# Kernel optimization log

Measured on AMD Instinct MI355X. Metric: run time of the kernel, lower is better.

## Reference

```python
import jax, jax.numpy as jnp
import numpy as np

SLOPE = 0.2  # leaky_relu_slope for both LVC block and kernel predictor (passed through)
DILATIONS = (1, 3, 9, 27)
HOP = 256
STRIDE = 8
IN_CH = 32
KSZ = 3  # conv_kernel_size


def conv1d(x, w, b, dilation=1, padding=0):
    # x: (B,C,T), w: (O,I,K) torch layout
    y = jax.lax.conv_general_dilated(
        x, w, window_strides=(1,), padding=[(padding, padding)],
        rhs_dilation=(dilation,), dimension_numbers=('NCH', 'OIH', 'NCH'))
    return y + b[None, :, None]


def conv_transpose1d(x, w, b, stride, padding, output_padding=0):
    # w: torch ConvTranspose1d layout (Cin, Cout, K)
    w_ = jnp.flip(w, -1).transpose(1, 0, 2)  # (Cout, Cin, K)
    K = w.shape[2]
    pad = (K - 1 - padding, K - 1 - padding + output_padding)
    y = jax.lax.conv_general_dilated(
        x, w_, window_strides=(1,), padding=[pad],
        lhs_dilation=(stride,), dimension_numbers=('NCH', 'OIH', 'NCH'))
    return y + b[None, :, None]


def lrelu(x, slope=SLOPE):
    return jnp.where(x >= 0, x, slope * x)


def location_variable_convolution(x, kernel, bias, hop):
    # x: (B,C,T), kernel: (B,C,O,k,L), bias: (B,O,L); T == L*hop; dilation==1 path
    B, C, T = x.shape
    _, _, O, k, L = kernel.shape
    pad = (k - 1) // 2
    xp = jnp.pad(x, ((0, 0), (0, 0), (pad, pad)))
    # gather per-segment sliding windows: (L, hop, k) index into time axis
    idx = (jnp.arange(L)[:, None, None] * hop
           + jnp.arange(hop)[None, :, None]
           + jnp.arange(k)[None, None, :])
    xw = xp[:, :, idx]  # (B, C, L, hop, k)
    o = jnp.einsum('bclsk,bcokl->bols', xw, kernel)  # (B, O, L, hop)
    o = o + bias[:, :, :, None]
    return o.reshape(B, O, L * hop)


def kernel_predictor(spec, kp_in_w, kp_in_b, rb_w1, rb_b1, rb_w2, rb_b2,
                     kern_w, kern_b, bias_w, bias_b):
    B, _, L = spec.shape
    h = conv1d(spec, kp_in_w, kp_in_b, padding=2)  # k=5, pad=2
    for i in range(3):  # num_blocks = 3
        r = h
        h = conv1d(h, rb_w1[i], rb_b1[i], padding=1)
        h = lrelu(h)
        h = conv1d(h, rb_w2[i], rb_b2[i], padding=1)
        h = lrelu(h) + r
    kh = conv1d(h, kern_w, kern_b, padding=1)
    bh = conv1d(h, bias_w, bias_b, padding=1)
    n_layers = len(DILATIONS)
    kernels = kh.reshape(B, n_layers, IN_CH, 2 * IN_CH, KSZ, L)
    biases = bh.reshape(B, n_layers, 2 * IN_CH, L)
    return kernels, biases


def reference(hidden_states, spectrogram, convt_w, convt_b, kp_in_w, kp_in_b,
              rb_w1, rb_b1, rb_w2, rb_b2, kern_w, kern_b, bias_w, bias_b,
              lvc_w, lvc_b):
    h = conv_transpose1d(hidden_states, convt_w, convt_b,
                         stride=STRIDE, padding=STRIDE // 2 + STRIDE % 2,
                         output_padding=STRIDE % 2)
    kernels, biases = kernel_predictor(spectrogram, kp_in_w, kp_in_b,
                                       rb_w1, rb_b1, rb_w2, rb_b2,
                                       kern_w, kern_b, bias_w, bias_b)
    for i, d in enumerate(DILATIONS):
        r = h
        h = lrelu(h)
        h = conv1d(h, lvc_w[i], lvc_b[i], dilation=d, padding=d * (KSZ - 1) // 2)
        h = lrelu(h)
        h = location_variable_convolution(h, kernels[:, i], biases[:, i], HOP)
        h = jax.nn.sigmoid(h[:, :IN_CH, :]) * jnp.tanh(h[:, IN_CH:, :]) + r
    return h


def setup_inputs() -> dict:
    key = jax.random.key(0)
    ks = jax.random.split(key, 12)
    B, COND, L, H = 4, 100, 256, 64
    T = L * HOP  # 65536 output samples
    s = jnp.float32(0.02)
    d = {}
    d['hidden_states'] = jax.random.normal(ks[0], (B, IN_CH, T // STRIDE), jnp.float32)
    d['spectrogram'] = jax.random.normal(ks[1], (B, COND, L), jnp.float32)
    d['convt_w'] = jax.random.normal(ks[2], (IN_CH, IN_CH, 2 * STRIDE), jnp.float32) * s
    d['convt_b'] = jnp.zeros((IN_CH,), jnp.float32)
    d['kp_in_w'] = jax.random.normal(ks[3], (H, COND, 5), jnp.float32) * s
    d['kp_in_b'] = jnp.zeros((H,), jnp.float32)
    d['rb_w1'] = jax.random.normal(ks[4], (3, H, H, 3), jnp.float32) * s
    d['rb_b1'] = jnp.zeros((3, H), jnp.float32)
    d['rb_w2'] = jax.random.normal(ks[5], (3, H, H, 3), jnp.float32) * s
    d['rb_b2'] = jnp.zeros((3, H), jnp.float32)
    KC = IN_CH * 2 * IN_CH * KSZ * len(DILATIONS)  # 24576
    d['kern_w'] = jax.random.normal(ks[6], (KC, H, 3), jnp.float32) * s
    d['kern_b'] = jnp.zeros((KC,), jnp.float32)
    BC = 2 * IN_CH * len(DILATIONS)  # 256
    d['bias_w'] = jax.random.normal(ks[7], (BC, H, 3), jnp.float32) * s
    d['bias_b'] = jnp.zeros((BC,), jnp.float32)
    d['lvc_w'] = jax.random.normal(ks[8], (len(DILATIONS), IN_CH, IN_CH, 3), jnp.float32) * s
    d['lvc_b'] = jnp.zeros((len(DILATIONS), IN_CH), jnp.float32)
    return d
```

## Files before the change

kernel.cpp:

```cpp
#include <hip/hip_runtime.h>
#include <math.h>

#define NB 4
#define T 65536
#define TIN 8192
#define LL 256
#define KCL 6144

__device__ __forceinline__ float lrelu_f(float v) { return v >= 0.f ? v : 0.2f * v; }

union Phase1LDS {
    struct { float xs[32][264]; float wm[64][128]; } cvt;
    struct { float hs[64][56]; float xsp[20][56]; float wt[192][68]; } trk;
};

__global__ void __launch_bounds__(512) phase1(
    const float* __restrict__ x, const float* __restrict__ cw,
    const float* __restrict__ cbias, float* __restrict__ hout,
    const float* __restrict__ spec,
    const float* __restrict__ kp_in_w, const float* __restrict__ kp_in_b,
    const float* __restrict__ rb_w1, const float* __restrict__ rb_b1,
    const float* __restrict__ rb_w2, const float* __restrict__ rb_b2,
    float* __restrict__ kp_h) {
    __shared__ Phase1LDS u;
    const int bid = blockIdx.x;
    const int tid = threadIdx.x;
    const int lane = tid & 63, wv = tid >> 6;

    if (bid < 264) {
        const int bx = bid % 33;
        const int rr = bid / 33;
        const int mtp = rr & 1;
        const int b = rr >> 1;
        const int s0base = bx * 256;
        float (*xs)[264] = u.cvt.xs;
        float (*wm)[128] = u.cvt.wm;

        const float* xb = x + (size_t)b * 32 * TIN;
        for (int idx = tid; idx < 32 * 64; idx += 512) {
            int c = idx >> 6, q = idx & 63;
            int p = s0base + q * 4;
            float4 v = (p + 3 < TIN) ? *(const float4*)(xb + c * TIN + p)
                                     : make_float4(0.f, 0.f, 0.f, 0.f);
            *(float4*)&xs[c][4 + 4 * q] = v;
        }
        if (tid < 32) {
            int p = s0base - 1;
            xs[tid][3] = (p >= 0) ? xb[tid * TIN + p] : 0.f;
        }
        for (int idx = tid; idx < 8192; idx += 512) {
            int i = idx >> 7, mm = idx & 127;
            int oo = mtp * 16 + (mm >> 3), k0 = mm & 7;
            wm[i][mm] = (i < 32) ? cw[i * 512 + oo * 16 + k0]
                                 : cw[(i - 32) * 512 + oo * 16 + k0 + 8];
        }
        __syncthreads();

        float acc[2][8][4];
#pragma unroll
        for (int ol = 0; ol < 2; ++ol) {
            float bo = cbias[mtp * 16 + wv * 2 + ol];
#pragma unroll
            for (int k0 = 0; k0 < 8; ++k0)
#pragma unroll
                for (int si = 0; si < 4; ++si) acc[ol][k0][si] = bo;
        }

        for (int c = 0; c < 32; ++c) {
            float xm1[4], x0[4];
#pragma unroll
            for (int si = 0; si < 4; ++si) {
                xm1[si] = xs[c][lane + si * 64 + 3];
                x0[si]  = xs[c][lane + si * 64 + 4];
            }
            float w0[16], w1[16];
#pragma unroll
            for (int q = 0; q < 4; ++q) {
                *(float4*)&w0[q * 4] = *(const float4*)&wm[c][wv * 16 + q * 4];
                *(float4*)&w1[q * 4] = *(const float4*)&wm[32 + c][wv * 16 + q * 4];
            }
#pragma unroll
            for (int ol = 0; ol < 2; ++ol)
#pragma unroll
                for (int k0 = 0; k0 < 8; ++k0)
#pragma unroll
                    for (int si = 0; si < 4; ++si)
                        acc[ol][k0][si] += x0[si] * w0[ol * 8 + k0] + xm1[si] * w1[ol * 8 + k0];
        }

#pragma unroll
        for (int ol = 0; ol < 2; ++ol) {
            float* ob = hout + ((size_t)b * 32 + mtp * 16 + wv * 2 + ol) * T;
#pragma unroll
            for (int si = 0; si < 4; ++si) {
                int tb = (s0base + lane + si * 64) * 8 - 4;
                if (tb >= 0 && tb < T)
                    *(float4*)(ob + tb) = make_float4(acc[ol][0][si], acc[ol][1][si],
                                                      acc[ol][2][si], acc[ol][3][si]);
                if (tb + 4 >= 0 && tb + 4 < T)
                    *(float4*)(ob + tb + 4) = make_float4(acc[ol][4][si], acc[ol][5][si],
                                                          acc[ol][6][si], acc[ol][7][si]);
            }
        }
        return;
    }

    const int tb = bid - 264;
    const int lq = tb & 7, b = tb >> 3;
    const int j = lane;
    const int oc0 = wv * 8;
    const int l0 = lq * 32;
    const int labs = l0 - 9 + j;
    const bool lvalid = (labs >= 0 && labs < 256);

    float (*hs)[56] = u.trk.hs;
    float (*xsp)[56] = u.trk.xsp;
    float (*wt)[68] = u.trk.wt;

    float pw[24];
    float px[3];

    auto pf_kpin = [&](int cc) {
#pragma unroll
        for (int t = 0; t < 13; ++t) {
            int idx = t * 512 + tid;
            pw[t] = 0.f;
            if (idx < 6400) pw[t] = kp_in_w[(size_t)(idx / 100) * 500 + cc * 100 + (idx % 100)];
        }
    };
    auto wr_kpin = [&]() {
#pragma unroll
        for (int t = 0; t < 13; ++t) {
            int idx = t * 512 + tid;
            if (idx < 6400) wt[idx % 100][idx / 100] = pw[t];
        }
    };
    auto pf_xsp = [&](int cc) {
#pragma unroll
        for (int t = 0; t < 3; ++t) {
            int idx = t * 512 + tid;
            px[t] = 0.f;
            if (idx < 1120) {
                int c = idx / 56, jj = idx - c * 56;
                int l = l0 - 9 + jj;
                if (l >= 0 && l < 256)
                    px[t] = spec[((size_t)b * 100 + cc * 20 + c) * LL + l];
            }
        }
    };
    auto wr_xsp = [&]() {
#pragma unroll
        for (int t = 0; t < 3; ++t) {
            int idx = t * 512 + tid;
            if (idx < 1120) xsp[idx / 56][idx % 56] = px[t];
        }
    };
    auto pf_w192 = [&](const float* src) {
#pragma unroll
        for (int t = 0; t < 24; ++t) pw[t] = src[t * 512 + tid];
    };
    auto wr_w192 = [&]() {
#pragma unroll
        for (int t = 0; t < 24; ++t) {
            int idx = t * 512 + tid;
            wt[idx % 192][idx / 192] = pw[t];
        }
    };
    auto conv64 = [&](int jlo, int jhi, const float* bptr, float* a) {
#pragma unroll
        for (int oi = 0; oi < 8; ++oi) a[oi] = bptr[oc0 + oi];
        if (j >= jlo && j < jhi) {
            for (int c = 0; c < 64; ++c) {
                float x0 = hs[c][j - 1], x1 = hs[c][j], x2 = hs[c][j + 1];
#pragma unroll
                for (int k = 0; k < 3; ++k) {
                    float xk = (k == 0) ? x0 : (k == 1) ? x1 : x2;
                    float w8[8];
                    *(float4*)&w8[0] = *(const float4*)&wt[c * 3 + k][oc0];
                    *(float4*)&w8[4] = *(const float4*)&wt[c * 3 + k][oc0 + 4];
#pragma unroll
                    for (int oi = 0; oi < 8; ++oi) a[oi] += xk * w8[oi];
                }
            }
        }
    };

    pf_kpin(0); pf_xsp(0);
    wr_kpin(); wr_xsp();
    __syncthreads();

    float acc[8];
#pragma unroll
    for (int oi = 0; oi < 8; ++oi) acc[oi] = kp_in_b[oc0 + oi];

    for (int cc = 0; cc < 5; ++cc) {
        if (cc < 4) { pf_kpin(cc + 1); pf_xsp(cc + 1); }
        else        { pf_w192(rb_w1); }
        if (j >= 2 && j < 48) {
            for (int c = 0; c < 20; ++c) {
                float x5[5];
#pragma unroll
                for (int u2 = 0; u2 < 5; ++u2) x5[u2] = xsp[c][j - 2 + u2];
#pragma unroll
                for (int k = 0; k < 5; ++k) {
                    float w8[8];
                    *(float4*)&w8[0] = *(const float4*)&wt[c * 5 + k][oc0];
                    *(float4*)&w8[4] = *(const float4*)&wt[c * 5 + k][oc0 + 4];
#pragma unroll
                    for (int oi = 0; oi < 8; ++oi) acc[oi] += x5[k] * w8[oi];
                }
            }
        }
        if (cc == 4 && j >= 2 && j < 48) {
#pragma unroll
            for (int oi = 0; oi < 8; ++oi) hs[oc0 + oi][j] = lvalid ? acc[oi] : 0.f;
        }
        __syncthreads();
        if (cc < 4) { wr_kpin(); wr_xsp(); }
        else        { wr_w192(); }
        __syncthreads();
    }

    for (int i = 0; i < 3; ++i) {
        const int jlo1 = 3 + 2 * i, jhi1 = 47 - 2 * i;
        const int jlo2 = jlo1 + 1, jhi2 = jhi1 - 1;
        float r[8];
        if (j >= jlo2 && j < jhi2) {
#pragma unroll
            for (int oi = 0; oi < 8; ++oi) r[oi] = hs[oc0 + oi][j];
        }
        pf_w192(rb_w2 + (size_t)i * 12288);
        float a1[8];
        conv64(jlo1, jhi1, rb_b1 + i * 64, a1);
        __syncthreads();
        if (j >= jlo1 && j < jhi1) {
#pragma unroll
            for (int oi = 0; oi < 8; ++oi) hs[oc0 + oi][j] = lvalid ? lrelu_f(a1[oi]) : 0.f;
        }
        wr_w192();
        __syncthreads();
        if (i < 2) pf_w192(rb_w1 + (size_t)(i + 1) * 12288);
        float a2[8];
        conv64(jlo2, jhi2, rb_b2 + i * 64, a2);
        __syncthreads();
        if (j >= jlo2 && j < jhi2) {
#pragma unroll
            for (int oi = 0; oi < 8; ++oi) hs[oc0 + oi][j] = lvalid ? (lrelu_f(a2[oi]) + r[oi]) : 0.f;
        }
        if (i < 2) wr_w192();
        __syncthreads();
    }

    for (int idx = tid; idx < 64 * 32; idx += 512) {
        int c = idx >> 5, jj = idx & 31;
        kp_h[((size_t)b * 64 + c) * LL + l0 + jj] = hs[c][9 + jj];
    }
}

__global__ void __launch_bounds__(256, 3) kern_head(const float* __restrict__ kp_h,
                                                    const float* __restrict__ kw,
                                                    const float* __restrict__ kb,
                                                    const float* __restrict__ bias_w,
                                                    const float* __restrict__ bias_b,
                                                    float* __restrict__ kh,
                                                    float* __restrict__ bh, int layer) {
    const int bx = blockIdx.x, b = blockIdx.y;
    const bool isbias = (bx >= 192);
    const int tid = threadIdx.x, lane = tid & 63, wv = tid >> 6;
    __shared__ float xs[32][264];
    __shared__ float ws[96][36];

    int g = 0, oc0 = 0, ci = 0, kk = 0, ocb0 = 0;
    const float* wsrc;
    size_t wrow0;
    int wstride;
    if (!isbias) {
        g = bx >> 1; oc0 = (bx & 1) * 32;
        ci = g / 3; kk = g - ci * 3;
        wsrc = kw + (size_t)layer * KCL * 192;
        wrow0 = (size_t)((ci * 64 + oc0) * 3 + kk) * 192;
        wstride = 576;
    } else {
        ocb0 = (bx - 192) * 32;
        wsrc = bias_w;
        wrow0 = (size_t)ocb0 * 192;
        wstride = 192;
    }

    float acc[8][4];
#pragma unroll
    for (int oi = 0; oi < 8; ++oi) {
        float bv = isbias ? bias_b[ocb0 + wv * 8 + oi]
                          : kb[layer * KCL + (ci * 64 + oc0 + wv * 8 + oi) * 3 + kk];
#pragma unroll
        for (int si = 0; si < 4; ++si) acc[oi][si] = bv;
    }

    for (int half = 0; half < 2; ++half) {
        const int hc0 = half * 32;
        __syncthreads();
        for (int idx = tid; idx < 32 * 64; idx += 256) {
            int c = idx >> 6, q = idx & 63;
            *(float4*)&xs[c][4 + 4 * q] =
                *(const float4*)(kp_h + ((size_t)b * 64 + hc0 + c) * LL + 4 * q);
        }
        if (tid < 32) { xs[tid][3] = 0.f; xs[tid][260] = 0.f; }
        for (int idx = tid; idx < 3072; idx += 256) {
            int ocl = idx / 96, jj = idx - ocl * 96;
            ws[jj][ocl] = wsrc[wrow0 + (size_t)ocl * wstride + hc0 * 3 + jj];
        }
        __syncthreads();
        for (int c = 0; c < 32; ++c) {
#pragma unroll
            for (int t = 0; t < 3; ++t) {
                float wv8[8];
                *(float4*)&wv8[0] = *(const float4*)&ws[c * 3 + t][wv * 8];
                *(float4*)&wv8[4] = *(const float4*)&ws[c * 3 + t][wv * 8 + 4];
                float xv[4];
#pragma unroll
                for (int si = 0; si < 4; ++si) xv[si] = xs[c][lane + si * 64 + t + 3];
#pragma unroll
                for (int oi = 0; oi < 8; ++oi)
#pragma unroll
                    for (int si = 0; si < 4; ++si)
                        acc[oi][si] += wv8[oi] * xv[si];
            }
        }
    }

    if (!isbias) {
#pragma unroll
        for (int si = 0; si < 4; ++si) {
            int l = lane + si * 64;
            float* op = kh + ((size_t)b * LL + l) * KCL + g * 64 + oc0 + wv * 8;
            *(float4*)(op)     = make_float4(acc[0][si], acc[1][si], acc[2][si], acc[3][si]);
            *(float4*)(op + 4) = make_float4(acc[4][si], acc[5][si], acc[6][si], acc[7][si]);
        }
    } else {
#pragma unroll
        for (int oi = 0; oi < 8; ++oi) {
            float* op = bh + ((size_t)b * 256 + ocb0 + wv * 8 + oi) * LL;
#pragma unroll
            for (int si = 0; si < 4; ++si)
                op[lane + si * 64] = acc[oi][si];
        }
    }
}

__global__ void __launch_bounds__(512, 4) layer_fused(
    const float* __restrict__ kh, const float* __restrict__ bh,
    const float* __restrict__ w, const float* __restrict__ bias,
    const float* __restrict__ hin, float* __restrict__ hout,
    int layer, int dil) {
    const int l = blockIdx.x, b = blockIdx.y;
    const int tid = threadIdx.x, lane = tid & 63, wv = tid >> 6;
    const int t0 = l * 256;
    __shared__ float xh[32][316];
    __shared__ float ks[KCL];
    __shared__ float ws[96][36];

    const float* hb = hin + (size_t)b * 32 * T;
    for (int idx = tid; idx < 32 * 64; idx += 512) {
        int c = idx >> 6, q = idx & 63;
        float4 v = *(const float4*)(hb + (size_t)c * T + t0 + 4 * q);
        *(float4*)&xh[c][32 + 4 * q] = make_float4(lrelu_f(v.x), lrelu_f(v.y),
                                                   lrelu_f(v.z), lrelu_f(v.w));
    }
    for (int idx = tid; idx < 32 * 60; idx += 512) {
        int c = idx / 60, r = idx - c * 60;
        int jj = (r < 32) ? r : (256 + r);
        int t = t0 + jj - 32;
        xh[c][jj] = (t >= 0 && t < T) ? lrelu_f(hb[(size_t)c * T + t]) : 0.f;
    }
    {
        const float4* kp = (const float4*)(kh + ((size_t)b * LL + l) * KCL);
        float4* kd = (float4*)ks;
        for (int idx = tid; idx < KCL / 4; idx += 512) kd[idx] = kp[idx];
    }
    for (int idx = tid; idx < 3072; idx += 512) {
        int oc = idx / 96, ck = idx - oc * 96;
        ws[ck][oc] = w[oc * 96 + ck];
    }
    __syncthreads();

    const int oc4 = wv * 4;
    float yv[5][4];
    {
        float a[5][4];
#pragma unroll
        for (int oi = 0; oi < 4; ++oi) {
            float bv = bias[oc4 + oi];
#pragma unroll
            for (int si = 0; si < 5; ++si) a[si][oi] = bv;
        }
        for (int c = 0; c < 32; ++c) {
#pragma unroll
            for (int k = 0; k < 3; ++k) {
                float4 wq = *(const float4*)&ws[c * 3 + k][oc4];
                float xv[5];
#pragma unroll
                for (int si = 0; si < 5; ++si) {
                    int col = lane + si * 64;
                    int colc = (col < 258) ? col : 257;
                    xv[si] = xh[c][colc + 31 + (k - 1) * dil];
                }
#pragma unroll
                for (int si = 0; si < 5; ++si) {
                    a[si][0] += xv[si] * wq.x;
                    a[si][1] += xv[si] * wq.y;
                    a[si][2] += xv[si] * wq.z;
                    a[si][3] += xv[si] * wq.w;
                }
            }
        }
#pragma unroll
        for (int si = 0; si < 5; ++si) {
            int t = t0 - 1 + lane + si * 64;
            bool tval = (t >= 0 && t < T);
#pragma unroll
            for (int oi = 0; oi < 4; ++oi)
                yv[si][oi] = tval ? lrelu_f(a[si][oi]) : 0.f;
        }
    }
    __syncthreads();

#pragma unroll
    for (int si = 0; si < 5; ++si) {
        int col = lane + si * 64;
        if (col < 258) {
#pragma unroll
            for (int oi = 0; oi < 4; ++oi) xh[oc4 + oi][col + 31] = yv[si][oi];
        }
    }
    __syncthreads();

    const int oc8 = (wv & 3) * 8;
    const int sh  = wv >> 2;
    float acc_a[8][2], acc_g[8][2];
#pragma unroll
    for (int oi = 0; oi < 8; ++oi) {
        float ba = bh[((size_t)b * 256 + layer * 64 + oc8 + oi) * LL + l];
        float bg = bh[((size_t)b * 256 + layer * 64 + 32 + oc8 + oi) * LL + l];
#pragma unroll
        for (int si = 0; si < 2; ++si) { acc_a[oi][si] = ba; acc_g[oi][si] = bg; }
    }

    for (int c = 0; c < 32; ++c) {
#pragma unroll
        for (int k = 0; k < 3; ++k) {
            const float* kr = ks + (c * 3 + k) * 64;
            float wa[8], wg[8];
            *(float4*)&wa[0] = *(const float4*)(kr + oc8);
            *(float4*)&wa[4] = *(const float4*)(kr + oc8 + 4);
            *(float4*)&wg[0] = *(const float4*)(kr + 32 + oc8);
            *(float4*)&wg[4] = *(const float4*)(kr + 32 + oc8 + 4);
            float xv2[2];
#pragma unroll
            for (int si = 0; si < 2; ++si) {
                int s = lane + (sh * 2 + si) * 64;
                xv2[si] = xh[c][s + k + 31];
            }
#pragma unroll
            for (int oi = 0; oi < 8; ++oi)
#pragma unroll
                for (int si = 0; si < 2; ++si) {
                    acc_a[oi][si] += wa[oi] * xv2[si];
                    acc_g[oi][si] += wg[oi] * xv2[si];
                }
        }
    }

#pragma unroll
    for (int oi = 0; oi < 8; ++oi) {
        const float* hip = hin + ((size_t)b * 32 + oc8 + oi) * T + t0;
        float* hop = hout + ((size_t)b * 32 + oc8 + oi) * T + t0;
#pragma unroll
        for (int si = 0; si < 2; ++si) {
            int s = lane + (sh * 2 + si) * 64;
            float a = acc_a[oi][si], g = acc_g[oi][si];
            float sg = 1.f / (1.f + __expf(-a));
            float th = tanhf(g);
            hop[s] = sg * th + hip[s];
        }
    }
}

extern "C" void kernel_launch(void* const* d_in, const int* in_sizes, int n_in,
                              void* d_out, int out_size, void* d_ws, size_t ws_size,
                              hipStream_t stream) {
    const float* hidden  = (const float*)d_in[0];
    const float* spec    = (const float*)d_in[1];
    const float* convt_w = (const float*)d_in[2];
    const float* convt_b = (const float*)d_in[3];
    const float* kp_in_w = (const float*)d_in[4];
    const float* kp_in_b = (const float*)d_in[5];
    const float* rb_w1   = (const float*)d_in[6];
    const float* rb_b1   = (const float*)d_in[7];
    const float* rb_w2   = (const float*)d_in[8];
    const float* rb_b2   = (const float*)d_in[9];
    const float* kern_w  = (const float*)d_in[10];
    const float* kern_b  = (const float*)d_in[11];
    const float* bias_w  = (const float*)d_in[12];
    const float* bias_b  = (const float*)d_in[13];
    const float* lvc_w   = (const float*)d_in[14];
    const float* lvc_b   = (const float*)d_in[15];

    float* wsp = (float*)d_ws;
    float* h_ws     = wsp;
    float* kh_layer = h_ws + (size_t)NB * 32 * T;
    float* bh       = kh_layer + (size_t)NB * LL * KCL;
    float* kp_h     = bh + (size_t)NB * 256 * LL;

    float* h0 = (float*)d_out;
    float* h1 = h_ws;

    phase1<<<dim3(296), 512, 0, stream>>>(hidden, convt_w, convt_b, h0,
                                          spec, kp_in_w, kp_in_b,
                                          rb_w1, rb_b1, rb_w2, rb_b2, kp_h);

    static const int dil[4] = {1, 3, 9, 27};
    float* hin = h0;
    float* hout = h1;
    for (int layer = 0; layer < 4; ++layer) {
        kern_head<<<dim3(layer == 0 ? 200 : 192, NB), 256, 0, stream>>>(
            kp_h, kern_w, kern_b, bias_w, bias_b, kh_layer, bh, layer);
        layer_fused<<<dim3(LL, NB), 512, 0, stream>>>(
            kh_layer, bh, lvc_w + (size_t)layer * 32 * 32 * 3, lvc_b + layer * 32,
            hin, hout, layer, dil[layer]);
        float* tmp = hin; hin = hout; hout = tmp;
    }
}
```

Measured before the change: 721.6 us.

## Pre-transpose weights in prep kernels and read them directly from global memory

Adds prep kernels that transpose the conv-transpose, kernel-predictor, residual-block, bias-head, LVC and per-layer kern_w weights into output-channel-contiguous layouts in workspace. The compute kernels then read these weights with wave-uniform global loads instead of staging them through LDS, and the wave index is made scalar with readfirstlane. This removes the LDS staging, its barriers and the strided gathers, but adds extra launches and a per-layer transpose pass over kern_w each call.

```diff
diff --git a/kernel.cpp b/kernel.cpp
--- a/kernel.cpp
+++ b/kernel.cpp
@@ -9,524 +9,550 @@
 
 __device__ __forceinline__ float lrelu_f(float v) { return v >= 0.f ? v : 0.2f * v; }
 
+__global__ void __launch_bounds__(256) prep1(
+    const float* __restrict__ bias_w, const float* __restrict__ rb_w1,
+    const float* __restrict__ rb_w2, const float* __restrict__ kp_in_w,
+    const float* __restrict__ convt_w, const float* __restrict__ lvc_w,
+    float* __restrict__ tbw, float* __restrict__ trb, float* __restrict__ tkpin,
+    float* __restrict__ tcvt, float* __restrict__ tlvc) {
+  __shared__ float t[64][193];
+  const int bid = blockIdx.x, tid = threadIdx.x;
+  if (bid < 10) {
+    const float* src; float* dst; int dstride, dcol;
+    if (bid < 6) {
+      int i = bid >> 1, which = bid & 1;
+      src = (which ? rb_w2 : rb_w1) + (size_t)i * 12288;
+      dst = trb + (size_t)bid * 12288; dstride = 64; dcol = 0;
+    } else {
+      int ob = bid - 6;
+      src = bias_w + (size_t)ob * 64 * 192;
+      dst = tbw; dstride = 256; dcol = ob * 64;
+    }
+    for (int idx = tid; idx < 64 * 192; idx += 256) {
+      int o = idx / 192, J = idx % 192;
+      t[o][J] = src[(size_t)o * 192 + J];
+    }
+    __syncthreads();
+    for (int idx = tid; idx < 64 * 192; idx += 256) {
+      int J = idx >> 6, o = idx & 63;
+      dst[(size_t)J * dstride + dcol + o] = t[o][J];
+    }
+  } else if (bid == 10) {
+    for (int idx = tid; idx < 500 * 64; idx += 256) {
+      int row = idx >> 6, o = idx & 63;
+      tkpin[idx] = kp_in_w[o * 500 + row];
+    }
+  } else if (bid == 11) {
+    for (int idx = tid; idx < 16384; idx += 256) {
+      int mtp = idx >> 13, r = idx & 8191, i = r >> 7, mm = r & 127;
+      int oo = mtp * 16 + (mm >> 3), k0 = mm & 7;
+      tcvt[idx] = (i < 32) ? convt_w[i * 512 + oo * 16 + k0]
+                           : convt_w[(i - 32) * 512 + oo * 16 + k0 + 8];
+    }
+  } else {
+    for (int idx = tid; idx < 12288; idx += 256) {
+      int layer = idx / 3072, r = idx % 3072, ck = r >> 5, o = r & 31;
+      tlvc[idx] = lvc_w[(size_t)layer * 3072 + o * 96 + ck];
+    }
+  }
+}
+
+__global__ void __launch_bounds__(256) prep_kern(const float* __restrict__ kern_w,
+                                                 float* __restrict__ tkwL, int layer) {
+  __shared__ float t[64][193];
+  const int g = blockIdx.x, tid = threadIdx.x;
+  const int ci = g / 3, kk = g % 3;
+  const float* src = kern_w + ((size_t)layer * KCL + ci * 192 + kk) * 192;
+  float* dst = tkwL + (size_t)g * 12288;
+  for (int idx = tid; idx < 64 * 192; idx += 256) {
+    int o = idx / 192, J = idx % 192;
+    t[o][J] = src[(size_t)o * 576 + J];
+  }
+  __syncthreads();
+  for (int idx = tid; idx < 64 * 192; idx += 256) {
+    int J = idx >> 6, o = idx & 63;
+    dst[(size_t)J * 64 + o] = t[o][J];
+  }
+}
+
 union Phase1LDS {
-    struct { float xs[32][264]; float wm[64][128]; } cvt;
-    struct { float hs[64][56]; float xsp[20][56]; float wt[192][68]; } trk;
+  struct { float xs[32][264]; } cvt;
+  struct { float hs[64][56]; float xsp[20][56]; } trk;
 };
 
 __global__ void __launch_bounds__(512) phase1(
-    const float* __restrict__ x, const float* __restrict__ cw,
+    const float* __restrict__ x, const float* __restrict__ tcvt,
     const float* __restrict__ cbias, float* __restrict__ hout,
     const float* __restrict__ spec,
-    const float* __restrict__ kp_in_w, const float* __restrict__ kp_in_b,
-    const float* __restrict__ rb_w1, const float* __restrict__ rb_b1,
-    const float* __restrict__ rb_w2, const float* __restrict__ rb_b2,
-    float* __restrict__ kp_h) {
-    __shared__ Phase1LDS u;
-    const int bid = blockIdx.x;
-    const int tid = threadIdx.x;
-    const int lane = tid & 63, wv = tid >> 6;
-
-    if (bid < 264) {
-        const int bx = bid % 33;
-        const int rr = bid / 33;
-        const int mtp = rr & 1;
-        const int b = rr >> 1;
-        const int s0base = bx * 256;
-        float (*xs)[264] = u.cvt.xs;
-        float (*wm)[128] = u.cvt.wm;
-
-        const float* xb = x + (size_t)b * 32 * TIN;
-        for (int idx = tid; idx < 32 * 64; idx += 512) {
-            int c = idx >> 6, q = idx & 63;
-            int p = s0base + q * 4;
-            float4 v = (p + 3 < TIN) ? *(const float4*)(xb + c * TIN + p)
-                                     : make_float4(0.f, 0.f, 0.f, 0.f);
-            *(float4*)&xs[c][4 + 4 * q] = v;
+    const float* __restrict__ tkpin, const float* __restrict__ kp_in_b,
+    const float* __restrict__ trb, const float* __restrict__ rb_b1,
+    const float* __restrict__ rb_b2, float* __restrict__ kp_h) {
+  __shared__ Phase1LDS u;
+  const int bid = blockIdx.x;
+  const int tid = threadIdx.x;
+  const int lane = tid & 63;
+  const int wvu = __builtin_amdgcn_readfirstlane(tid >> 6);
+
+  if (bid < 264) {
+    const int bx = bid % 33;
+    const int rr = bid / 33;
+    const int mtp = rr & 1;
+    const int b = rr >> 1;
+    const int s0base = bx * 256;
+    float (*xs)[264] = u.cvt.xs;
+
+    const float* xb = x + (size_t)b * 32 * TIN;
+    for (int idx = tid; idx < 32 * 64; idx += 512) {
+      int c = idx >> 6, q = idx & 63;
+      int p = s0base + q * 4;
+      float4 v = (p + 3 < TIN) ? *(const float4*)(xb + c * TIN + p)
+                               : make_float4(0.f, 0.f, 0.f, 0.f);
+      *(float4*)&xs[c][4 + 4 * q] = v;
+    }
+    if (tid < 32) {
+      int p = s0base - 1;
+      xs[tid][3] = (p >= 0) ? xb[tid * TIN + p] : 0.f;
+    }
+    __syncthreads();
+
+    float acc[2][8][4];
+#pragma unroll
+    for (int ol = 0; ol < 2; ++ol) {
+      float bo = cbias[mtp * 16 + wvu * 2 + ol];
+#pragma unroll
+      for (int k0 = 0; k0 < 8; ++k0)
+#pragma unroll
+        for (int si = 0; si < 4; ++si) acc[ol][k0][si] = bo;
+    }
+
+    const float* wcb = tcvt + (size_t)mtp * 8192 + wvu * 16;
+    for (int c = 0; c < 32; ++c) {
+      float w0[16], w1[16];
+#pragma unroll
+      for (int q = 0; q < 16; ++q) {
+        w0[q] = wcb[c * 128 + q];
+        w1[q] = wcb[(32 + c) * 128 + q];
+      }
+      float xm1[4], x0[4];
+#pragma unroll
+      for (int si = 0; si < 4; ++si) {
+        xm1[si] = xs[c][lane + si * 64 + 3];
+        x0[si]  = xs[c][lane + si * 64 + 4];
+      }
+#pragma unroll
+      for (int ol = 0; ol < 2; ++ol)
+#pragma unroll
+        for (int k0 = 0; k0 < 8; ++k0)
+#pragma unroll
+          for (int si = 0; si < 4; ++si)
+            acc[ol][k0][si] += x0[si] * w0[ol * 8 + k0] + xm1[si] * w1[ol * 8 + k0];
+    }
+
+#pragma unroll
+    for (int ol = 0; ol < 2; ++ol) {
+      float* ob = hout + ((size_t)b * 32 + mtp * 16 + wvu * 2 + ol) * T;
+#pragma unroll
+      for (int si = 0; si < 4; ++si) {
+        int tb = (s0base + lane + si * 64) * 8 - 4;
+        if (tb >= 0 && tb < T)
+          *(float4*)(ob + tb) = make_float4(acc[ol][0][si], acc[ol][1][si],
+                                            acc[ol][2][si], acc[ol][3][si]);
+        if (tb + 4 >= 0 && tb + 4 < T)
+          *(float4*)(ob + tb + 4) = make_float4(acc[ol][4][si], acc[ol][5][si],
+                                                acc[ol][6][si], acc[ol][7][si]);
+      }
+    }
+    return;
+  }
+
+  const int tb = bid - 264;
+  const int lq = tb & 7, b = tb >> 3;
+  const int j = lane;
+  const int oc0 = wvu * 8;
+  const int l0 = lq * 32;
+  const int labs = l0 - 9 + j;
+  const bool lvalid = (labs >= 0 && labs < 256);
+
+  float (*hs)[56] = u.trk.hs;
+  float (*xsp)[56] = u.trk.xsp;
+
+  float px[3];
+  auto pf_xsp = [&](int cc) {
+#pragma unroll
+    for (int t = 0; t < 3; ++t) {
+      int idx = t * 512 + tid;
+      px[t] = 0.f;
+      if (idx < 1120) {
+        int c = idx / 56, jj = idx - c * 56;
+        int l = l0 - 9 + jj;
+        if (l >= 0 && l < 256)
+          px[t] = spec[((size_t)b * 100 + cc * 20 + c) * LL + l];
+      }
+    }
+  };
+  auto wr_xsp = [&]() {
+#pragma unroll
+    for (int t = 0; t < 3; ++t) {
+      int idx = t * 512 + tid;
+      if (idx < 1120) xsp[idx / 56][idx % 56] = px[t];
+    }
+  };
+  auto conv64 = [&](int jlo, int jhi, const float* bptr, const float* wconv, float* a) {
+#pragma unroll
+    for (int oi = 0; oi < 8; ++oi) a[oi] = bptr[oc0 + oi];
+    if (j >= jlo && j < jhi) {
+      for (int c = 0; c < 64; ++c) {
+        const float* wp = wconv + (size_t)(c * 3) * 64 + oc0;
+        float w0[8], w1[8], w2[8];
+#pragma unroll
+        for (int oi = 0; oi < 8; ++oi) {
+          w0[oi] = wp[oi];
+          w1[oi] = wp[64 + oi];
+          w2[oi] = wp[128 + oi];
         }
-        if (tid < 32) {
-            int p = s0base - 1;
-            xs[tid][3] = (p >= 0) ? xb[tid * TIN + p] : 0.f;
+        float x0 = hs[c][j - 1], x1 = hs[c][j], x2 = hs[c][j + 1];
+#pragma unroll
+        for (int oi = 0; oi < 8; ++oi)
+          a[oi] += x0 * w0[oi] + x1 * w1[oi] + x2 * w2[oi];
+      }
+    }
+  };
+
+  pf_xsp(0);
+  wr_xsp();
+  __syncthreads();
+
+  float acc[8];
+#pragma unroll
+  for (int oi = 0; oi < 8; ++oi) acc[oi] = kp_in_b[oc0 + oi];
+
+  for (int cc = 0; cc < 5; ++cc) {
+    if (cc < 4) pf_xsp(cc + 1);
+    if (j >= 2 && j < 48) {
+      for (int c = 0; c < 20; ++c) {
+        float x5[5];
+#pragma unroll
+        for (int u2 = 0; u2 < 5; ++u2) x5[u2] = xsp[c][j - 2 + u2];
+        const float* wp = tkpin + (size_t)((cc * 20 + c) * 5) * 64 + oc0;
+#pragma unroll
+        for (int k = 0; k < 5; ++k) {
+          float w8[8];
+#pragma unroll
+          for (int oi = 0; oi < 8; ++oi) w8[oi] = wp[k * 64 + oi];
+#pragma unroll
+          for (int oi = 0; oi < 8; ++oi) acc[oi] += x5[k] * w8[oi];
         }
-        for (int idx = tid; idx < 8192; idx += 512) {
-            int i = idx >> 7, mm = idx & 127;
-            int oo = mtp * 16 + (mm >> 3), k0 = mm & 7;
-            wm[i][mm] = (i < 32) ? cw[i * 512 + oo * 16 + k0]
-                                 : cw[(i - 32) * 512 + oo * 16 + k0 + 8];
-        }
-        __syncthreads();
-
-        float acc[2][8][4];
-#pragma unroll
-        for (int ol = 0; ol < 2; ++ol) {
-            float bo = cbias[mtp * 16 + wv * 2 + ol];
-#pragma unroll
-            for (int k0 = 0; k0 < 8; ++k0)
-#pragma unroll
-                for (int si = 0; si < 4; ++si) acc[ol][k0][si] = bo;
-        }
-
-        for (int c = 0; c < 32; ++c) {
-            float xm1[4], x0[4];
-#pragma unroll
-            for (int si = 0; si < 4; ++si) {
-                xm1[si] = xs[c][lane + si * 64 + 3];
-                x0[si]  = xs[c][lane + si * 64 + 4];
-            }
-            float w0[16], w1[16];
-#pragma unroll
-            for (int q = 0; q < 4; ++q) {
-                *(float4*)&w0[q * 4] = *(const float4*)&wm[c][wv * 16 + q * 4];
-                *(float4*)&w1[q * 4] = *(const float4*)&wm[32 + c][wv * 16 + q * 4];
-            }
-#pragma unroll
-            for (int ol = 0; ol < 2; ++ol)
-#pragma unroll
-                for (int k0 = 0; k0 < 8; ++k0)
-#pragma unroll
-                    for (int si = 0; si < 4; ++si)
-                        acc[ol][k0][si] += x0[si] * w0[ol * 8 + k0] + xm1[si] * w1[ol * 8 + k0];
-        }
-
-#pragma unroll
-        for (int ol = 0; ol < 2; ++ol) {
-            float* ob = hout + ((size_t)b * 32 + mtp * 16 + wv * 2 + ol) * T;
-#pragma unroll
-            for (int si = 0; si < 4; ++si) {
-                int tb = (s0base + lane + si * 64) * 8 - 4;
-                if (tb >= 0 && tb < T)
-                    *(float4*)(ob + tb) = make_float4(acc[ol][0][si], acc[ol][1][si],
-                                                      acc[ol][2][si], acc[ol][3][si]);
-                if (tb + 4 >= 0 && tb + 4 < T)
-                    *(float4*)(ob + tb + 4) = make_float4(acc[ol][4][si], acc[ol][5][si],
-                                                          acc[ol][6][si], acc[ol][7][si]);
-            }
-        }
-        return;
-    }
-
-    const int tb = bid - 264;
-    const int lq = tb & 7, b = tb >> 3;
-    const int j = lane;
-    const int oc0 = wv * 8;
-    const int l0 = lq * 32;
-    const int labs = l0 - 9 + j;
-    const bool lvalid = (labs >= 0 && labs < 256);
-
-    float (*hs)[56] = u.trk.hs;
-    float (*xsp)[56] = u.trk.xsp;
-    float (*wt)[68] = u.trk.wt;
-
-    float pw[24];
-    float px[3];
-
-    auto pf_kpin = [&](int cc) {
-#pragma unroll
-        for (int t = 0; t < 13; ++t) {
-            int idx = t * 512 + tid;
-            pw[t] = 0.f;
-            if (idx < 6400) pw[t] = kp_in_w[(size_t)(idx / 100) * 500 + cc * 100 + (idx % 100)];
-        }
-    };
-    auto wr_kpin = [&]() {
-#pragma unroll
-        for (int t = 0; t < 13; ++t) {
-            int idx = t * 512 + tid;
-            if (idx < 6400) wt[idx % 100][idx / 100] = pw[t];
-        }
-    };
-    auto pf_xsp = [&](int cc) {
-#pragma unroll
-        for (int t = 0; t < 3; ++t) {
-            int idx = t * 512 + tid;
-            px[t] = 0.f;
-            if (idx < 1120) {
-                int c = idx / 56, jj = idx - c * 56;
-                int l = l0 - 9 + jj;
-                if (l >= 0 && l < 256)
-                    px[t] = spec[((size_t)b * 100 + cc * 20 + c) * LL + l];
-            }
-        }
-    };
-    auto wr_xsp = [&]() {
-#pragma unroll
-        for (int t = 0; t < 3; ++t) {
-            int idx = t * 512 + tid;
-            if (idx < 1120) xsp[idx / 56][idx % 56] = px[t];
-        }
-    };
-    auto pf_w192 = [&](const float* src) {
-#pragma unroll
-        for (int t = 0; t < 24; ++t) pw[t] = src[t * 512 + tid];
-    };
-    auto wr_w192 = [&]() {
-#pragma unroll
-        for (int t = 0; t < 24; ++t) {
-            int idx = t * 512 + tid;
-            wt[idx % 192][idx / 192] = pw[t];
-        }
-    };
-    auto conv64 = [&](int jlo, int jhi, const float* bptr, float* a) {
-#pragma unroll
-        for (int oi = 0; oi < 8; ++oi) a[oi] = bptr[oc0 + oi];
-        if (j >= jlo && j < jhi) {
-            for (int c = 0; c < 64; ++c) {
-                float x0 = hs[c][j - 1], x1 = hs[c][j], x2 = hs[c][j + 1];
-#pragma unroll
-                for (int k = 0; k < 3; ++k) {
-                    float xk = (k == 0) ? x0 : (k == 1) ? x1 : x2;
-                    float w8[8];
-                    *(float4*)&w8[0] = *(const float4*)&wt[c * 3 + k][oc0];
-                    *(float4*)&w8[4] = *(const float4*)&wt[c * 3 + k][oc0 + 4];
-#pragma unroll
-                    for (int oi = 0; oi < 8; ++oi) a[oi] += xk * w8[oi];
-                }
-            }
-        }
-    };
-
-    pf_kpin(0); pf_xsp(0);
-    wr_kpin(); wr_xsp();
-    __syncthreads();
-
-    float acc[8];
-#pragma unroll
-    for (int oi = 0; oi < 8; ++oi) acc[oi] = kp_in_b[oc0 + oi];
-
-    for (int cc = 0; cc < 5; ++cc) {
-        if (cc < 4) { pf_kpin(cc + 1); pf_xsp(cc + 1); }
-        else        { pf_w192(rb_w1); }
-        if (j >= 2 && j < 48) {
-            for (int c = 0; c < 20; ++c) {
-                float x5[5];
-#pragma unroll
-                for (int u2 = 0; u2 < 5; ++u2) x5[u2] = xsp[c][j - 2 + u2];
-#pragma unroll
-                for (int k = 0; k < 5; ++k) {
-                    float w8[8];
-                    *(float4*)&w8[0] = *(const float4*)&wt[c * 5 + k][oc0];
-                    *(float4*)&w8[4] = *(const float4*)&wt[c * 5 + k][oc0 + 4];
-#pragma unroll
-                    for (int oi = 0; oi < 8; ++oi) acc[oi] += x5[k] * w8[oi];
-                }
-            }
-        }
-        if (cc == 4 && j >= 2 && j < 48) {
-#pragma unroll
-            for (int oi = 0; oi < 8; ++oi) hs[oc0 + oi][j] = lvalid ? acc[oi] : 0.f;
-        }
-        __syncthreads();
-        if (cc < 4) { wr_kpin(); wr_xsp(); }
-        else        { wr_w192(); }
-        __syncthreads();
-    }
-
-    for (int i = 0; i < 3; ++i) {
-        const int jlo1 = 3 + 2 * i, jhi1 = 47 - 2 * i;
-        const int jlo2 = jlo1 + 1, jhi2 = jhi1 - 1;
-        float r[8];
-        if (j >= jlo2 && j < jhi2) {
-#pragma unroll
-            for (int oi = 0; oi < 8; ++oi) r[oi] = hs[oc0 + oi][j];
-        }
-        pf_w192(rb_w2 + (size_t)i * 12288);
-        float a1[8];
-        conv64(jlo1, jhi1, rb_b1 + i * 64, a1);
-        __syncthreads();
-        if (j >= jlo1 && j < jhi1) {
-#pragma unroll
-            for (int oi = 0; oi < 8; ++oi) hs[oc0 + oi][j] = lvalid ? lrelu_f(a1[oi]) : 0.f;
-        }
-        wr_w192();
-        __syncthreads();
-        if (i < 2) pf_w192(rb_w1 + (size_t)(i + 1) * 12288);
-        float a2[8];
-        conv64(jlo2, jhi2, rb_b2 + i * 64, a2);
-        __syncthreads();
-        if (j >= jlo2 && j < jhi2) {
-#pragma unroll
-            for (int oi = 0; oi < 8; ++oi) hs[oc0 + oi][j] = lvalid ? (lrelu_f(a2[oi]) + r[oi]) : 0.f;
-        }
-        if (i < 2) wr_w192();
-        __syncthreads();
-    }
-
-    for (int idx = tid; idx < 64 * 32; idx += 512) {
-        int c = idx >> 5, jj = idx & 31;
-        kp_h[((size_t)b * 64 + c) * LL + l0 + jj] = hs[c][9 + jj];
-    }
+      }
+    }
+    if (cc == 4 && j >= 2 && j < 48) {
+#pragma unroll
+      for (int oi = 0; oi < 8; ++oi) hs[oc0 + oi][j] = lvalid ? acc[oi] : 0.f;
+    }
+    __syncthreads();
+    if (cc < 4) wr_xsp();
+    __syncthreads();
+  }
+
+  for (int i = 0; i < 3; ++i) {
+    const int jlo1 = 3 + 2 * i, jhi1 = 47 - 2 * i;
+    const int jlo2 = jlo1 + 1, jhi2 = jhi1 - 1;
+    float r[8];
+    if (j >= jlo2 && j < jhi2) {
+#pragma unroll
+      for (int oi = 0; oi < 8; ++oi) r[oi] = hs[oc0 + oi][j];
+    }
+    float a1[8];
+    conv64(jlo1, jhi1, rb_b1 + i * 64, trb + (size_t)(2 * i) * 12288, a1);
+    __syncthreads();
+    if (j >= jlo1 && j < jhi1) {
+#pragma unroll
+      for (int oi = 0; oi < 8; ++oi) hs[oc0 + oi][j] = lvalid ? lrelu_f(a1[oi]) : 0.f;
+    }
+    __syncthreads();
+    float a2[8];
+    conv64(jlo2, jhi2, rb_b2 + i * 64, trb + (size_t)(2 * i + 1) * 12288, a2);
+    __syncthreads();
+    if (j >= jlo2 && j < jhi2) {
+#pragma unroll
+      for (int oi = 0; oi < 8; ++oi) hs[oc0 + oi][j] = lvalid ? (lrelu_f(a2[oi]) + r[oi]) : 0.f;
+    }
+    __syncthreads();
+  }
+
+  for (int idx = tid; idx < 64 * 32; idx += 512) {
+    int c = idx >> 5, jj = idx & 31;
+    kp_h[((size_t)b * 64 + c) * LL + l0 + jj] = hs[c][9 + jj];
+  }
 }
 
-__global__ void __launch_bounds__(256, 3) kern_head(const float* __restrict__ kp_h,
-                                                    const float* __restrict__ kw,
+__global__ void __launch_bounds__(256, 4) kern_head(const float* __restrict__ kp_h,
+                                                    const float* __restrict__ tkwL,
                                                     const float* __restrict__ kb,
-                                                    const float* __restrict__ bias_w,
+                                                    const float* __restrict__ tbw,
                                                     const float* __restrict__ bias_b,
                                                     float* __restrict__ kh,
                                                     float* __restrict__ bh, int layer) {
-    const int bx = blockIdx.x, b = blockIdx.y;
-    const bool isbias = (bx >= 192);
-    const int tid = threadIdx.x, lane = tid & 63, wv = tid >> 6;
-    __shared__ float xs[32][264];
-    __shared__ float ws[96][36];
-
-    int g = 0, oc0 = 0, ci = 0, kk = 0, ocb0 = 0;
-    const float* wsrc;
-    size_t wrow0;
-    int wstride;
-    if (!isbias) {
-        g = bx >> 1; oc0 = (bx & 1) * 32;
-        ci = g / 3; kk = g - ci * 3;
-        wsrc = kw + (size_t)layer * KCL * 192;
-        wrow0 = (size_t)((ci * 64 + oc0) * 3 + kk) * 192;
-        wstride = 576;
-    } else {
-        ocb0 = (bx - 192) * 32;
-        wsrc = bias_w;
-        wrow0 = (size_t)ocb0 * 192;
-        wstride = 192;
-    }
-
-    float acc[8][4];
+  const int bx = blockIdx.x, b = blockIdx.y;
+  const bool isbias = (bx >= 192);
+  const int tid = threadIdx.x, lane = tid & 63;
+  const int wvu = __builtin_amdgcn_readfirstlane(tid >> 6);
+  __shared__ float xs[32][264];
+
+  int g = 0, oc0 = 0, ci = 0, kk = 0, ocb0 = 0;
+  const float* wbase;
+  int wstride;
+  if (!isbias) {
+    g = bx >> 1; oc0 = (bx & 1) * 32;
+    ci = g / 3; kk = g - ci * 3;
+    wbase = tkwL + (size_t)g * 12288 + oc0 + wvu * 8;
+    wstride = 64;
+  } else {
+    ocb0 = (bx - 192) * 32;
+    wbase = tbw + ocb0 + wvu * 8;
+    wstride = 256;
+  }
+
+  float acc[8][4];
+#pragma unroll
+  for (int oi = 0; oi < 8; ++oi) {
+    float bv = isbias ? bias_b[ocb0 + wvu * 8 + oi]
+                      : kb[layer * KCL + (ci * 64 + oc0 + wvu * 8 + oi) * 3 + kk];
+#pragma unroll
+    for (int q = 0; q < 4; ++q) acc[oi][q] = bv;
+  }
+
+  for (int half = 0; half < 2; ++half) {
+    const int hc0 = half * 32;
+    __syncthreads();
+    for (int idx = tid; idx < 32 * 64; idx += 256) {
+      int c = idx >> 6, q = idx & 63;
+      *(float4*)&xs[c][4 + 4 * q] =
+          *(const float4*)(kp_h + ((size_t)b * 64 + hc0 + c) * LL + 4 * q);
+    }
+    if (tid < 32) { xs[tid][3] = 0.f; xs[tid][260] = 0.f; }
+    __syncthreads();
+    const float* wb2 = wbase + (size_t)(hc0 * 3) * wstride;
+    for (int c = 0; c < 32; ++c) {
+      float w[3][8];
+#pragma unroll
+      for (int t3 = 0; t3 < 3; ++t3)
+#pragma unroll
+        for (int oi = 0; oi < 8; ++oi)
+          w[t3][oi] = wb2[(size_t)(c * 3 + t3) * wstride + oi];
+      float4 xa = *(const float4*)&xs[c][4 * lane];
+      float4 xm = *(const float4*)&xs[c][4 + 4 * lane];
+      float4 xb = *(const float4*)&xs[c][8 + 4 * lane];
+      float xx[6] = {xa.w, xm.x, xm.y, xm.z, xm.w, xb.x};
+#pragma unroll
+      for (int t3 = 0; t3 < 3; ++t3)
+#pragma unroll
+        for (int oi = 0; oi < 8; ++oi)
+#pragma unroll
+          for (int q = 0; q < 4; ++q)
+            acc[oi][q] += w[t3][oi] * xx[q + t3];
+    }
+  }
+
+  if (!isbias) {
+#pragma unroll
+    for (int q = 0; q < 4; ++q) {
+      int l = 4 * lane + q;
+      float* op = kh + ((size_t)b * LL + l) * KCL + g * 64 + oc0 + wvu * 8;
+      *(float4*)(op)     = make_float4(acc[0][q], acc[1][q], acc[2][q], acc[3][q]);
+      *(float4*)(op + 4) = make_float4(acc[4][q], acc[5][q], acc[6][q], acc[7][q]);
+    }
+  } else {
 #pragma unroll
     for (int oi = 0; oi < 8; ++oi) {
-        float bv = isbias ? bias_b[ocb0 + wv * 8 + oi]
-                          : kb[layer * KCL + (ci * 64 + oc0 + wv * 8 + oi) * 3 + kk];
-#pragma unroll
-        for (int si = 0; si < 4; ++si) acc[oi][si] = bv;
-    }
-
-    for (int half = 0; half < 2; ++half) {
-        const int hc0 = half * 32;
-        __syncthreads();
-        for (int idx = tid; idx < 32 * 64; idx += 256) {
-            int c = idx >> 6, q = idx & 63;
-            *(float4*)&xs[c][4 + 4 * q] =
-                *(const float4*)(kp_h + ((size_t)b * 64 + hc0 + c) * LL + 4 * q);
-        }
-        if (tid < 32) { xs[tid][3] = 0.f; xs[tid][260] = 0.f; }
-        for (int idx = tid; idx < 3072; idx += 256) {
-            int ocl = idx / 96, jj = idx - ocl * 96;
-            ws[jj][ocl] = wsrc[wrow0 + (size_t)ocl * wstride + hc0 * 3 + jj];
-        }
-        __syncthreads();
-        for (int c = 0; c < 32; ++c) {
-#pragma unroll
-            for (int t = 0; t < 3; ++t) {
-                float wv8[8];
-                *(float4*)&wv8[0] = *(const float4*)&ws[c * 3 + t][wv * 8];
-                *(float4*)&wv8[4] = *(const float4*)&ws[c * 3 + t][wv * 8 + 4];
-                float xv[4];
-#pragma unroll
-                for (int si = 0; si < 4; ++si) xv[si] = xs[c][lane + si * 64 + t + 3];
-#pragma unroll
-                for (int oi = 0; oi < 8; ++oi)
-#pragma unroll
-                    for (int si = 0; si < 4; ++si)
-                        acc[oi][si] += wv8[oi] * xv[si];
-            }
-        }
-    }
-
-    if (!isbias) {
-#pragma unroll
-        for (int si = 0; si < 4; ++si) {
-            int l = lane + si * 64;
-            float* op = kh + ((size_t)b * LL + l) * KCL + g * 64 + oc0 + wv * 8;
-            *(float4*)(op)     = make_float4(acc[0][si], acc[1][si], acc[2][si], acc[3][si]);
-            *(float4*)(op + 4) = make_float4(acc[4][si], acc[5][si], acc[6][si], acc[7][si]);
-        }
-    } else {
-#pragma unroll
-        for (int oi = 0; oi < 8; ++oi) {
-            float* op = bh + ((size_t)b * 256 + ocb0 + wv * 8 + oi) * LL;
-#pragma unroll
-            for (int si = 0; si < 4; ++si)
-                op[lane + si * 64] = acc[oi][si];
-        }
-    }
+      float* op = bh + ((size_t)b * 256 + ocb0 + wvu * 8 + oi) * LL + 4 * lane;
+      *(float4*)op = make_float4(acc[oi][0], acc[oi][1], acc[oi][2], acc[oi][3]);
+    }
+  }
 }
 
-__global__ void __launch_bounds__(512, 4) layer_fused(
+__global__ void __launch_bounds__(512, 8) layer_fused(
     const float* __restrict__ kh, const float* __restrict__ bh,
-    const float* __restrict__ w, const float* __restrict__ bias,
+    const float* __restrict__ wT, const float* __restrict__ bias,
     const float* __restrict__ hin, float* __restrict__ hout,
     int layer, int dil) {
-    const int l = blockIdx.x, b = blockIdx.y;
-    const int tid = threadIdx.x, lane = tid & 63, wv = tid >> 6;
-    const int t0 = l * 256;
-    __shared__ float xh[32][316];
-    __shared__ float ks[KCL];
-    __shared__ float ws[96][36];
-
-    const float* hb = hin + (size_t)b * 32 * T;
-    for (int idx = tid; idx < 32 * 64; idx += 512) {
-        int c = idx >> 6, q = idx & 63;
-        float4 v = *(const float4*)(hb + (size_t)c * T + t0 + 4 * q);
-        *(float4*)&xh[c][32 + 4 * q] = make_float4(lrelu_f(v.x), lrelu_f(v.y),
-                                                   lrelu_f(v.z), lrelu_f(v.w));
-    }
-    for (int idx = tid; idx < 32 * 60; idx += 512) {
-        int c = idx / 60, r = idx - c * 60;
-        int jj = (r < 32) ? r : (256 + r);
-        int t = t0 + jj - 32;
-        xh[c][jj] = (t >= 0 && t < T) ? lrelu_f(hb[(size_t)c * T + t]) : 0.f;
-    }
-    {
-        const float4* kp = (const float4*)(kh + ((size_t)b * LL + l) * KCL);
-        float4* kd = (float4*)ks;
-        for (int idx = tid; idx < KCL / 4; idx += 512) kd[idx] = kp[idx];
-    }
-    for (int idx = tid; idx < 3072; idx += 512) {
-        int oc = idx / 96, ck = idx - oc * 96;
-        ws[ck][oc] = w[oc * 96 + ck];
-    }
-    __syncthreads();
-
-    const int oc4 = wv * 4;
-    float yv[5][4];
-    {
-        float a[5][4];
-#pragma unroll
-        for (int oi = 0; oi < 4; ++oi) {
-            float bv = bias[oc4 + oi];
-#pragma unroll
-            for (int si = 0; si < 5; ++si) a[si][oi] = bv;
+  const int l = blockIdx.x, b = blockIdx.y;
+  const int tid = threadIdx.x, lane = tid & 63;
+  const int wvu = __builtin_amdgcn_readfirstlane(tid >> 6);
+  const int t0 = l * 256;
+  __shared__ float xh[32][316];
+
+  const float* hb = hin + (size_t)b * 32 * T;
+  for (int idx = tid; idx < 32 * 64; idx += 512) {
+    int c = idx >> 6, q = idx & 63;
+    float4 v = *(const float4*)(hb + (size_t)c * T + t0 + 4 * q);
+    *(float4*)&xh[c][32 + 4 * q] = make_float4(lrelu_f(v.x), lrelu_f(v.y),
+                                               lrelu_f(v.z), lrelu_f(v.w));
+  }
+  for (int idx = tid; idx < 32 * 60; idx += 512) {
+    int c = idx / 60, r = idx - c * 60;
+    int jj = (r < 32) ? r : (256 + r);
+    int t = t0 + jj - 32;
+    xh[c][jj] = (t >= 0 && t < T) ? lrelu_f(hb[(size_t)c * T + t]) : 0.f;
+  }
+  __syncthreads();
+
+  const int oc4 = wvu * 4;
+  float yv[5][4];
+  {
+    float a[5][4];
+#pragma unroll
+    for (int oi = 0; oi < 4; ++oi) {
+      float bv = bias[oc4 + oi];
+#pragma unroll
+      for (int si = 0; si < 5; ++si) a[si][oi] = bv;
+    }
+    for (int c = 0; c < 32; ++c) {
+#pragma unroll
+      for (int k = 0; k < 3; ++k) {
+        const float* wp = wT + (size_t)(c * 3 + k) * 32 + oc4;
+        float wq0 = wp[0], wq1 = wp[1], wq2 = wp[2], wq3 = wp[3];
+        float xv[5];
+#pragma unroll
+        for (int si = 0; si < 5; ++si) {
+          int col = lane + si * 64;
+          int colc = (col < 258) ? col : 257;
+          xv[si] = xh[c][colc + 31 + (k - 1) * dil];
         }
-        for (int c = 0; c < 32; ++c) {
-#pragma unroll
-            for (int k = 0; k < 3; ++k) {
-                float4 wq = *(const float4*)&ws[c * 3 + k][oc4];
-                float xv[5];
-#pragma unroll
-                for (int si = 0; si < 5; ++si) {
-                    int col = lane + si * 64;
-                    int colc = (col < 258) ? col : 257;
-                    xv[si] = xh[c][colc + 31 + (k - 1) * dil];
-                }
-#pragma unroll
-                for (int si = 0; si < 5; ++si) {
-                    a[si][0] += xv[si] * wq.x;
-                    a[si][1] += xv[si] * wq.y;
-                    a[si][2] += xv[si] * wq.z;
-                    a[si][3] += xv[si] * wq.w;
-                }
-            }
+#pragma unroll
+        for (int si = 0; si < 5; ++si) {
+          a[si][0] += xv[si] * wq0;
+          a[si][1] += xv[si] * wq1;
+          a[si][2] += xv[si] * wq2;
+          a[si][3] += xv[si] * wq3;
         }
-#pragma unroll
-        for (int si = 0; si < 5; ++si) {
-            int t = t0 - 1 + lane + si * 64;
-            bool tval = (t >= 0 && t < T);
-#pragma unroll
-            for (int oi = 0; oi < 4; ++oi)
-                yv[si][oi] = tval ? lrelu_f(a[si][oi]) : 0.f;
+      }
+    }
+#pragma unroll
+    for (int si = 0; si < 5; ++si) {
+      int t = t0 - 1 + lane + si * 64;
+      bool tval = (t >= 0 && t < T);
+#pragma unroll
+      for (int oi = 0; oi < 4; ++oi)
+        yv[si][oi] = tval ? lrelu_f(a[si][oi]) : 0.f;
+    }
+  }
+  __syncthreads();
+
+#pragma unroll
+  for (int si = 0; si < 5; ++si) {
+    int col = lane + si * 64;
+    if (col < 258) {
+#pragma unroll
+      for (int oi = 0; oi < 4; ++oi) xh[oc4 + oi][col + 31] = yv[si][oi];
+    }
+  }
+  __syncthreads();
+
+  const int oc8 = (wvu & 3) * 8;
+  const int sh  = wvu >> 2;
+  const float* krbase = kh + ((size_t)b * LL + l) * KCL;
+  float acc_a[8][2], acc_g[8][2];
+#pragma unroll
+  for (int oi = 0; oi < 8; ++oi) {
+    float ba = bh[((size_t)b * 256 + layer * 64 + oc8 + oi) * LL + l];
+    float bg = bh[((size_t)b * 256 + layer * 64 + 32 + oc8 + oi) * LL + l];
+#pragma unroll
+    for (int si = 0; si < 2; ++si) { acc_a[oi][si] = ba; acc_g[oi][si] = bg; }
+  }
+
+  for (int c = 0; c < 32; ++c) {
+#pragma unroll
+    for (int k = 0; k < 3; ++k) {
+      const float* kr = krbase + (size_t)(c * 3 + k) * 64;
+      float wa[8], wg[8];
+#pragma unroll
+      for (int oi = 0; oi < 8; ++oi) {
+        wa[oi] = kr[oc8 + oi];
+        wg[oi] = kr[32 + oc8 + oi];
+      }
+      float xv2[2];
+#pragma unroll
+      for (int si = 0; si < 2; ++si) {
+        int s = lane + (sh * 2 + si) * 64;
+        xv2[si] = xh[c][s + k + 31];
+      }
+#pragma unroll
+      for (int oi = 0; oi < 8; ++oi)
+#pragma unroll
+        for (int si = 0; si < 2; ++si) {
+          acc_a[oi][si] += wa[oi] * xv2[si];
+          acc_g[oi][si] += wg[oi] * xv2[si];
         }
     }
-    __syncthreads();
-
-#pragma unroll
-    for (int si = 0; si < 5; ++si) {
-        int col = lane + si * 64;
-        if (col < 258) {
-#pragma unroll
-            for (int oi = 0; oi < 4; ++oi) xh[oc4 + oi][col + 31] = yv[si][oi];
-        }
-    }
-    __syncthreads();
-
-    const int oc8 = (wv & 3) * 8;
-    const int sh  = wv >> 2;
-    float acc_a[8][2], acc_g[8][2];
-#pragma unroll
-    for (int oi = 0; oi < 8; ++oi) {
-        float ba = bh[((size_t)b * 256 + layer * 64 + oc8 + oi) * LL + l];
-        float bg = bh[((size_t)b * 256 + layer * 64 + 32 + oc8 + oi) * LL + l];
-#pragma unroll
-        for (int si = 0; si < 2; ++si) { acc_a[oi][si] = ba; acc_g[oi][si] = bg; }
-    }
-
-    for (int c = 0; c < 32; ++c) {
-#pragma unroll
-        for (int k = 0; k < 3; ++k) {
-            const float* kr = ks + (c * 3 + k) * 64;
-            float wa[8], wg[8];
-            *(float4*)&wa[0] = *(const float4*)(kr + oc8);
-            *(float4*)&wa[4] = *(const float4*)(kr + oc8 + 4);
-            *(float4*)&wg[0] = *(const float4*)(kr + 32 + oc8);
-            *(float4*)&wg[4] = *(const float4*)(kr + 32 + oc8 + 4);
-            float xv2[2];
-#pragma unroll
-            for (int si = 0; si < 2; ++si) {
-                int s = lane + (sh * 2 + si) * 64;
-                xv2[si] = xh[c][s + k + 31];
-            }
-#pragma unroll
-            for (int oi = 0; oi < 8; ++oi)
-#pragma unroll
-                for (int si = 0; si < 2; ++si) {
-                    acc_a[oi][si] += wa[oi] * xv2[si];
-                    acc_g[oi][si] += wg[oi] * xv2[si];
-                }
-        }
-    }
-
-#pragma unroll
-    for (int oi = 0; oi < 8; ++oi) {
-        const float* hip = hin + ((size_t)b * 32 + oc8 + oi) * T + t0;
-        float* hop = hout + ((size_t)b * 32 + oc8 + oi) * T + t0;
-#pragma unroll
-        for (int si = 0; si < 2; ++si) {
-            int s = lane + (sh * 2 + si) * 64;
-            float a = acc_a[oi][si], g = acc_g[oi][si];
-            float sg = 1.f / (1.f + __expf(-a));
-            float th = tanhf(g);
-            hop[s] = sg * th + hip[s];
-        }
-    }
+  }
+
+#pragma unroll
+  for (int oi = 0; oi < 8; ++oi) {
+    const float* hip = hin + ((size_t)b * 32 + oc8 + oi) * T + t0;
+    float* hop = hout + ((size_t)b * 32 + oc8 + oi) * T + t0;
+#pragma unroll
+    for (int si = 0; si < 2; ++si) {
+      int s = lane + (sh * 2 + si) * 64;
+      float a = acc_a[oi][si], g = acc_g[oi][si];
+      float sg = 1.f / (1.f + __expf(-a));
+      float th = tanhf(g);
+      hop[s] = sg * th + hip[s];
+    }
+  }
 }
 
 extern "C" void kernel_launch(void* const* d_in, const int* in_sizes, int n_in,
                               void* d_out, int out_size, void* d_ws, size_t ws_size,
                               hipStream_t stream) {
-    const float* hidden  = (const float*)d_in[0];
-    const float* spec    = (const float*)d_in[1];
-    const float* convt_w = (const float*)d_in[2];
-    const float* convt_b = (const float*)d_in[3];
-    const float* kp_in_w = (const float*)d_in[4];
-    const float* kp_in_b = (const float*)d_in[5];
-    const float* rb_w1   = (const float*)d_in[6];
-    const float* rb_b1   = (const float*)d_in[7];
-    const float* rb_w2   = (const float*)d_in[8];
-    const float* rb_b2   = (const float*)d_in[9];
-    const float* kern_w  = (const float*)d_in[10];
-    const float* kern_b  = (const float*)d_in[11];
-    const float* bias_w  = (const float*)d_in[12];
-    const float* bias_b  = (const float*)d_in[13];
-    const float* lvc_w   = (const float*)d_in[14];
-    const float* lvc_b   = (const float*)d_in[15];
-
-    float* wsp = (float*)d_ws;
-    float* h_ws     = wsp;
-    float* kh_layer = h_ws + (size_t)NB * 32 * T;
-    float* bh       = kh_layer + (size_t)NB * LL * KCL;
-    float* kp_h     = bh + (size_t)NB * 256 * LL;
-
-    float* h0 = (float*)d_out;
-    float* h1 = h_ws;
-
-    phase1<<<dim3(296), 512, 0, stream>>>(hidden, convt_w, convt_b, h0,
-                                          spec, kp_in_w, kp_in_b,
-                                          rb_w1, rb_b1, rb_w2, rb_b2, kp_h);
-
-    static const int dil[4] = {1, 3, 9, 27};
-    float* hin = h0;
-    float* hout = h1;
-    for (int layer = 0; layer < 4; ++layer) {
-        kern_head<<<dim3(layer == 0 ? 200 : 192, NB), 256, 0, stream>>>(
-            kp_h, kern_w, kern_b, bias_w, bias_b, kh_layer, bh, layer);
-        layer_fused<<<dim3(LL, NB), 512, 0, stream>>>(
-            kh_layer, bh, lvc_w + (size_t)layer * 32 * 32 * 3, lvc_b + layer * 32,
-            hin, hout, layer, dil[layer]);
-        float* tmp = hin; hin = hout; hout = tmp;
-    }
+  const float* hidden  = (const float*)d_in[0];
+  const float* spec    = (const float*)d_in[1];
+  const float* convt_w = (const float*)d_in[2];
+  const float* convt_b = (const float*)d_in[3];
+  const float* kp_in_w = (const float*)d_in[4];
+  const float* kp_in_b = (const float*)d_in[5];
+  const float* rb_w1   = (const float*)d_in[6];
+  const float* rb_b1   = (const float*)d_in[7];
+  const float* rb_w2   = (const float*)d_in[8];
+  const float* rb_b2   = (const float*)d_in[9];
+  const float* kern_w  = (const float*)d_in[10];
+  const float* kern_b  = (const float*)d_in[11];
+  const float* bias_w  = (const float*)d_in[12];
+  const float* bias_b  = (const float*)d_in[13];
+  const float* lvc_w   = (const float*)d_in[14];
+  const float* lvc_b   = (const float*)d_in[15];
+
+  float* wsp = (float*)d_ws;
+  float* h_ws     = wsp;
+  float* kh_layer = h_ws + (size_t)NB * 32 * T;
+  float* bh       = kh_layer + (size_t)NB * LL * KCL;
+  float* kp_h     = bh + (size_t)NB * 256 * LL;
+  float* tkwL     = kp_h + (size_t)NB * 64 * LL;
+  float* tbw      = tkwL + (size_t)96 * 192 * 64;
+  float* trb      = tbw + (size_t)192 * 256;
+  float* tkpin    = trb + (size_t)6 * 192 * 64;
+  float* tcvt     = tkpin + (size_t)500 * 64;
+  float* tlvc     = tcvt + (size_t)2 * 64 * 128;
+
+  float* h0 = (float*)d_out;
+  float* h1 = h_ws;
+
+  prep1<<<dim3(13), 256, 0, stream>>>(bias_w, rb_w1, rb_w2, kp_in_w, convt_w, lvc_w,
+                                      tbw, trb, tkpin, tcvt, tlvc);
+
+  phase1<<<dim3(296), 512, 0, stream>>>(hidden, tcvt, convt_b, h0,
+                                        spec, tkpin, kp_in_b,
+                                        trb, rb_b1, rb_b2, kp_h);
+
+  static const int dil[4] = {1, 3, 9, 27};
+  float* hin = h0;
+  float* hout = h1;
+  for (int layer = 0; layer < 4; ++layer) {
+    prep_kern<<<dim3(96), 256, 0, stream>>>(kern_w, tkwL, layer);
+    kern_head<<<dim3(layer == 0 ? 200 : 192, NB), 256, 0, stream>>>(
+        kp_h, tkwL, kern_b, tbw, bias_b, kh_layer, bh, layer);
+    layer_fused<<<dim3(LL, NB), 512, 0, stream>>>(
+        kh_layer, bh, tlvc + (size_t)layer * 3072, lvc_b + layer * 32,
+        hin, hout, layer, dil[layer]);
+    float* tmp = hin; hin = hout; hout = tmp;
+  }
 }
```

New measurement: 772.2 us. +7.0%, slower.
